# Kernel optimization log

Measured on AMD Instinct MI355X. Metric: run time of the kernel, lower is better.

Reference implementation:

```python
import jax, jax.numpy as jnp
import numpy as np

E = 8   # num_experts
K = 2   # top-k


def setup_inputs() -> dict:
    key = jax.random.key(0)
    ks = jax.random.split(key, 6)
    B, S, D, F = 4, 2048, 1024, 4096
    s_d = 1.0 / np.sqrt(D).astype(np.float32)
    s_f = 1.0 / np.sqrt(F).astype(np.float32)
    return {
        "x": jax.random.normal(ks[0], (B, S, D), jnp.float32),
        "ln_w": jnp.ones((D,), jnp.float32),                                 # RMSNorm weight
        "Wg": jax.random.normal(ks[1], (D, E), jnp.float32) * s_d,           # gating
        "bg": jnp.zeros((E,), jnp.float32),
        "W1a": jax.random.normal(ks[2], (E, D, F), jnp.float32) * s_d,       # stacked expert params
        "b1a": jnp.zeros((E, F), jnp.float32),
        "W1b": jax.random.normal(ks[3], (E, D, F), jnp.float32) * s_d,
        "b1b": jnp.zeros((E, F), jnp.float32),
        "W2": jax.random.normal(ks[4], (E, F, D), jnp.float32) * s_f,
        "b2": jnp.zeros((E, D), jnp.float32),
    }


def reference(x, ln_w, Wg, bg, W1a, b1a, W1b, b1b, W2, b2):
    B, S, D = x.shape
    eps = jnp.finfo(x.dtype).eps  # torch nn.RMSNorm default eps = finfo(dtype).eps
    # RMSNorm
    xn = x * jax.lax.rsqrt(jnp.mean(x * x, axis=-1, keepdims=True) + eps) * ln_w
    # gating -> top-k -> softmax over the k selected logits
    logits = xn @ Wg + bg                       # [B,S,E]
    vals, idx = jax.lax.top_k(logits, K)        # [B,S,K]
    topk_w = jax.nn.softmax(vals, axis=-1)      # [B,S,K]
    # combined per-expert gate weight per token (0 for unselected experts)
    we = jnp.sum(jax.nn.one_hot(idx, E, dtype=x.dtype) * topk_w[..., None], axis=-2)  # [B,S,E]

    T = B * S
    xf = xn.reshape(T, D)
    wef = we.reshape(T, E).T                    # [E,T], scanned per-expert

    def step(acc, params):
        W1a_e, b1a_e, W1b_e, b1b_e, W2_e, b2_e, w_e = params
        a = xf @ W1a_e + b1a_e                  # [T,F]
        b = xf @ W1b_e + b1b_e                  # [T,F]
        y = (jax.nn.silu(a) * b) @ W2_e + b2_e  # [T,D]
        return acc + w_e[:, None] * y, None

    out0 = jnp.zeros_like(xf)
    out, _ = jax.lax.scan(step, out0, (W1a, b1a, W1b, b1b, W2, b2, wef))
    return out.reshape(B, S, D)
```

## Files before the change

kernel.cpp:

```cpp
#include <hip/hip_runtime.h>
#include <hip/hip_bf16.h>
#include <cstdint>
#include <cstddef>

#define T_TOK 8192
#define DDIM  1024
#define FDIM  4096
#define NEXP  8
#define NSLOT (T_TOK*2)
#define BM    128
#define MAXTILE 136

typedef float  f32x4  __attribute__((ext_vector_type(4)));
typedef short  bf16x8 __attribute__((ext_vector_type(8)));
typedef unsigned short u16;

#define XN_OFF   ((size_t)0)
#define H_OFF    ((size_t)16777216)
#define META     ((size_t)(16777216+134217728))
#define CNT_OFF  (META + 0)
#define OFF_OFF  (META + 64)
#define NT_OFF   (META + 128)
#define TE_OFF   (META + 256)
#define TS_OFF   (META + 1024)
#define TR_OFF   (META + 1792)
#define EK_OFF   (META + 4096)
#define RK_OFF   (EK_OFF + 65536)
#define WK_OFF   (RK_OFF + 65536)
#define PT_OFF   (WK_OFF + 65536)
#define PW_OFF   (PT_OFF + 65536)
#define WT1A_OFF ((size_t)152 << 20)
#define WT1B_OFF (WT1A_OFF + ((size_t)64 << 20))
#define WT2_OFF  (WT1B_OFF + ((size_t)64 << 20))
#define WS_BIG   (WT2_OFF  + ((size_t)64 << 20))

__device__ __forceinline__ u16 f2bf(float f) {
    uint32_t x = __float_as_uint(f);
    x += 0x7fffu + ((x >> 16) & 1u);
    return (u16)(x >> 16);
}

__device__ __forceinline__ void gload_lds16(const u16* g, u16* l) {
    __builtin_amdgcn_global_load_lds(
        (const __attribute__((address_space(1))) unsigned int*)g,
        (__attribute__((address_space(3))) unsigned int*)l, 16, 0, 0);
}

__global__ __launch_bounds__(256) void k_rms_gate(
    const float* __restrict__ x, const float* __restrict__ lnw,
    const float* __restrict__ Wg, const float* __restrict__ bg,
    u16* __restrict__ xn, int* __restrict__ counts,
    int* __restrict__ ek, int* __restrict__ rk, float* __restrict__ wk)
{
    const int t = blockIdx.x;
    const int tid = threadIdx.x;
    const int wid = tid >> 6, lane = tid & 63;

    const float4 v = *(const float4*)(x + (size_t)t * DDIM + tid * 4);
    float ss = v.x * v.x + v.y * v.y + v.z * v.z + v.w * v.w;
    #pragma unroll
    for (int o = 32; o; o >>= 1) ss += __shfl_down(ss, o);

    __shared__ float s_red[4];
    __shared__ float s_lg[4][8];
    if (lane == 0) s_red[wid] = ss;
    __syncthreads();
    const float tot = s_red[0] + s_red[1] + s_red[2] + s_red[3];
    const float rms = rsqrtf(tot * (1.0f / DDIM) + 1.1920929e-7f);

    const float4 lw = *(const float4*)(lnw + tid * 4);
    float xv[4] = { v.x * rms * lw.x, v.y * rms * lw.y,
                    v.z * rms * lw.z, v.w * rms * lw.w };
    ushort4 xb;
    xb.x = f2bf(xv[0]); xb.y = f2bf(xv[1]); xb.z = f2bf(xv[2]); xb.w = f2bf(xv[3]);
    *(ushort4*)(xn + (size_t)t * DDIM + tid * 4) = xb;

    float lg[8];
    #pragma unroll
    for (int e = 0; e < 8; e++) lg[e] = 0.f;
    #pragma unroll
    for (int j = 0; j < 4; j++) {
        const float4 g0 = *(const float4*)(Wg + (size_t)(tid * 4 + j) * 8);
        const float4 g1 = *(const float4*)(Wg + (size_t)(tid * 4 + j) * 8 + 4);
        lg[0] += xv[j] * g0.x; lg[1] += xv[j] * g0.y;
        lg[2] += xv[j] * g0.z; lg[3] += xv[j] * g0.w;
        lg[4] += xv[j] * g1.x; lg[5] += xv[j] * g1.y;
        lg[6] += xv[j] * g1.z; lg[7] += xv[j] * g1.w;
    }
    #pragma unroll
    for (int e = 0; e < 8; e++) {
        #pragma unroll
        for (int o = 32; o; o >>= 1) lg[e] += __shfl_down(lg[e], o);
    }
    if (lane == 0) {
        #pragma unroll
        for (int e = 0; e < 8; e++) s_lg[wid][e] = lg[e];
    }
    __syncthreads();
    if (tid == 0) {
        float l[8];
        #pragma unroll
        for (int e = 0; e < 8; e++)
            l[e] = s_lg[0][e] + s_lg[1][e] + s_lg[2][e] + s_lg[3][e] + bg[e];
        int i0 = 0; float v0 = l[0];
        for (int e = 1; e < 8; e++) if (l[e] > v0) { v0 = l[e]; i0 = e; }
        int i1 = -1; float v1 = -3.4e38f;
        for (int e = 0; e < 8; e++) if (e != i0 && l[e] > v1) { v1 = l[e]; i1 = e; }
        const float w0 = 1.f / (1.f + __expf(v1 - v0));
        const float w1 = 1.f - w0;
        const int r0 = atomicAdd(&counts[i0], 1);
        const int r1 = atomicAdd(&counts[i1], 1);
        ek[t * 2]     = i0; rk[t * 2]     = r0; wk[t * 2]     = w0;
        ek[t * 2 + 1] = i1; rk[t * 2 + 1] = r1; wk[t * 2 + 1] = w1;
    }
}

__global__ void k_plan(const int* __restrict__ counts, int* __restrict__ offs,
                       int* __restrict__ ntile, int* __restrict__ tE,
                       int* __restrict__ tS, int* __restrict__ tR)
{
    if (threadIdx.x != 0 || blockIdx.x != 0) return;
    int off = 0, n = 0;
    for (int e = 0; e < NEXP; e++) {
        offs[e] = off;
        const int c = counts[e];
        for (int m = 0; m < c && n < MAXTILE; m += BM) {
            tE[n] = e; tS[n] = off + m; tR[n] = min(BM, c - m); n++;
        }
        off += c;
    }
    *ntile = n;
}

__global__ __launch_bounds__(256) void k_scatter(
    const int* __restrict__ ek, const int* __restrict__ rk,
    const float* __restrict__ wk, const int* __restrict__ offs,
    int* __restrict__ pt, float* __restrict__ pw)
{
    const int i = blockIdx.x * 256 + threadIdx.x;
    const int e = ek[i];
    const int slot = offs[e] + rk[i];
    pt[slot] = i >> 1;
    pw[slot] = wk[i];
}

__global__ __launch_bounds__(256) void k_transpose(
    const float* __restrict__ src, u16* __restrict__ dst, int R, int C)
{
    __shared__ u16 tile[64][72];
    const int e  = blockIdx.z;
    const int r0 = blockIdx.y * 64;
    const int c0 = blockIdx.x * 64;
    const int t  = threadIdx.x;
    const float* s = src + (size_t)e * R * C;
    u16* d         = dst + (size_t)e * R * C;

    const int lr = t >> 4;
    const int lc = (t & 15) * 4;
    #pragma unroll
    for (int i = 0; i < 4; i++) {
        const int r = lr + i * 16;
        const float4 v = *(const float4*)(s + (size_t)(r0 + r) * C + c0 + lc);
        tile[lc + 0][r] = f2bf(v.x);
        tile[lc + 1][r] = f2bf(v.y);
        tile[lc + 2][r] = f2bf(v.z);
        tile[lc + 3][r] = f2bf(v.w);
    }
    __syncthreads();
    const int wc = t >> 3;
    const int wr = (t & 7) * 8;
    #pragma unroll
    for (int i = 0; i < 2; i++) {
        const int c = wc + i * 32;
        const uint4 v = *(const uint4*)&tile[c][wr];
        *(uint4*)(d + (size_t)(c0 + c) * R + r0 + wr) = v;
    }
}

__global__ __launch_bounds__(256, 2) void k_gemm1_t(
    const u16* __restrict__ xn, const int* __restrict__ pt, const float* __restrict__ pw,
    const u16* __restrict__ wt1a, const float* __restrict__ b1a,
    const u16* __restrict__ wt1b, const float* __restrict__ b1b,
    const int* __restrict__ ntile, const int* __restrict__ tE,
    const int* __restrict__ tS, const int* __restrict__ tR,
    u16* __restrict__ h)
{
    const int bx = blockIdx.x;
    if (bx >= *ntile) return;
    const int e = tE[bx], slot0 = tS[bx], rows = tR[bx];
    const int f0 = blockIdx.y * 64;
    const int tid = threadIdx.x;

    __shared__ u16 lds[128 * 32 + 2 * 64 * 32];
    u16* ldsA  = lds;
    u16* ldsWa = lds + 128 * 32;
    u16* ldsWb = lds + 128 * 32 + 64 * 32;

    const int rA = tid >> 2, cA = tid & 3;
    const int tok0 = pt[slot0 + min(rA,      rows - 1)];
    const int tok1 = pt[slot0 + min(rA + 64, rows - 1)];
    const u16* gA0 = xn + (size_t)tok0 * DDIM + cA * 8;
    const u16* gA1 = xn + (size_t)tok1 * DDIM + cA * 8;
    const u16* gWa = wt1a + ((size_t)e * FDIM + f0 + rA) * DDIM + cA * 8;
    const u16* gWb = wt1b + ((size_t)e * FDIM + f0 + rA) * DDIM + cA * 8;
    u16* dA0 = ldsA  + tid * 8;
    u16* dA1 = ldsA  + 2048 + tid * 8;
    u16* dWa = ldsWa + tid * 8;
    u16* dWb = ldsWb + tid * 8;

    const int wid = tid >> 6, lane = tid & 63;
    const int wm = wid & 1, wn = wid >> 1;
    const int ln = lane & 15, q = lane >> 4;

    f32x4 accA[4][2], accB[4][2];
    #pragma unroll
    for (int i = 0; i < 4; i++)
        #pragma unroll
        for (int j = 0; j < 2; j++) {
            accA[i][j] = (f32x4){0.f, 0.f, 0.f, 0.f};
            accB[i][j] = (f32x4){0.f, 0.f, 0.f, 0.f};
        }

    for (int k0 = 0; k0 < DDIM; k0 += 32) {
        __syncthreads();
        gload_lds16(gA0 + k0, dA0);
        gload_lds16(gA1 + k0, dA1);
        gload_lds16(gWa + k0, dWa);
        gload_lds16(gWb + k0, dWb);
        __syncthreads();

        bf16x8 af[4], ba[2], bb[2];
        #pragma unroll
        for (int i = 0; i < 4; i++)
            af[i] = *(const bf16x8*)(ldsA + (wm * 64 + i * 16 + ln) * 32 + q * 8);
        #pragma unroll
        for (int j = 0; j < 2; j++) {
            ba[j] = *(const bf16x8*)(ldsWa + (wn * 32 + j * 16 + ln) * 32 + q * 8);
            bb[j] = *(const bf16x8*)(ldsWb + (wn * 32 + j * 16 + ln) * 32 + q * 8);
        }
        #pragma unroll
        for (int i = 0; i < 4; i++)
            #pragma unroll
            for (int j = 0; j < 2; j++) {
                accA[i][j] = __builtin_amdgcn_mfma_f32_16x16x32_bf16(af[i], ba[j], accA[i][j], 0, 0, 0);
                accB[i][j] = __builtin_amdgcn_mfma_f32_16x16x32_bf16(af[i], bb[j], accB[i][j], 0, 0, 0);
            }
    }

    #pragma unroll
    for (int i = 0; i < 4; i++) {
        const int mb = wm * 64 + i * 16 + q * 4;
        #pragma unroll
        for (int j = 0; j < 2; j++) {
            const int fg = f0 + wn * 32 + j * 16 + ln;
            const float bav = b1a[e * FDIM + fg];
            const float bbv = b1b[e * FDIM + fg];
            #pragma unroll
            for (int r = 0; r < 4; r++) {
                const int m = mb + r;
                if (m < rows) {
                    const float a = accA[i][j][r] + bav;
                    const float b = accB[i][j][r] + bbv;
                    const float s = a / (1.f + __expf(-a));
                    const float hv = pw[slot0 + m] * s * b;
                    h[(size_t)(slot0 + m) * FDIM + fg] = f2bf(hv);
                }
            }
        }
    }
}

__global__ __launch_bounds__(256, 2) void k_gemm2_t(
    const u16* __restrict__ h, const int* __restrict__ pt, const float* __restrict__ pw,
    const u16* __restrict__ wt2, const float* __restrict__ b2,
    const int* __restrict__ ntile, const int* __restrict__ tE,
    const int* __restrict__ tS, const int* __restrict__ tR,
    float* __restrict__ out)
{
    const int bx = blockIdx.x;
    if (bx >= *ntile) return;
    const int e = tE[bx], slot0 = tS[bx], rows = tR[bx];
    const int n0 = blockIdx.y * 128;
    const int tid = threadIdx.x;

    __shared__ u16 lds[2 * 128 * 32];
    u16* ldsA = lds;
    u16* ldsW = lds + 128 * 32;

    const int rA = tid >> 2, cA = tid & 3;
    const int r0c = min(rA,      rows - 1);
    const int r1c = min(rA + 64, rows - 1);
    const u16* gA0 = h + (size_t)(slot0 + r0c) * FDIM + cA * 8;
    const u16* gA1 = h + (size_t)(slot0 + r1c) * FDIM + cA * 8;
    const u16* gW0 = wt2 + ((size_t)e * DDIM + n0 + rA)      * FDIM + cA * 8;
    const u16* gW1 = wt2 + ((size_t)e * DDIM + n0 + rA + 64) * FDIM + cA * 8;
    u16* dA0 = ldsA + tid * 8;
    u16* dA1 = ldsA + 2048 + tid * 8;
    u16* dW0 = ldsW + tid * 8;
    u16* dW1 = ldsW + 2048 + tid * 8;

    const int wid = tid >> 6, lane = tid & 63;
    const int wm = wid & 1, wn = wid >> 1;
    const int ln = lane & 15, q = lane >> 4;

    f32x4 acc[4][4];
    #pragma unroll
    for (int i = 0; i < 4; i++)
        #pragma unroll
        for (int j = 0; j < 4; j++) acc[i][j] = (f32x4){0.f, 0.f, 0.f, 0.f};

    for (int k0 = 0; k0 < FDIM; k0 += 32) {
        __syncthreads();
        gload_lds16(gA0 + k0, dA0);
        gload_lds16(gA1 + k0, dA1);
        gload_lds16(gW0 + k0, dW0);
        gload_lds16(gW1 + k0, dW1);
        __syncthreads();

        bf16x8 af[4], bf[4];
        #pragma unroll
        for (int i = 0; i < 4; i++)
            af[i] = *(const bf16x8*)(ldsA + (wm * 64 + i * 16 + ln) * 32 + q * 8);
        #pragma unroll
        for (int j = 0; j < 4; j++)
            bf[j] = *(const bf16x8*)(ldsW + (wn * 64 + j * 16 + ln) * 32 + q * 8);
        #pragma unroll
        for (int i = 0; i < 4; i++)
            #pragma unroll
            for (int j = 0; j < 4; j++)
                acc[i][j] = __builtin_amdgcn_mfma_f32_16x16x32_bf16(af[i], bf[j], acc[i][j], 0, 0, 0);
    }

    #pragma unroll
    for (int i = 0; i < 4; i++) {
        const int mb = wm * 64 + i * 16 + q * 4;
        #pragma unroll
        for (int j = 0; j < 4; j++) {
            const int d = n0 + wn * 64 + j * 16 + ln;
            const float b2v = b2[e * DDIM + d];
            #pragma unroll
            for (int r = 0; r < 4; r++) {
                const int m = mb + r;
                if (m < rows) {
                    const int slot = slot0 + m;
                    const int tok = pt[slot];
                    const float val = acc[i][j][r] + pw[slot] * b2v;
                    atomicAdd(out + (size_t)tok * DDIM + d, val);
                }
            }
        }
    }
}


__global__ __launch_bounds__(256, 2) void k_gemm1(
    const u16* __restrict__ xn, const int* __restrict__ pt, const float* __restrict__ pw,
    const float* __restrict__ W1a, const float* __restrict__ b1a,
    const float* __restrict__ W1b, const float* __restrict__ b1b,
    const int* __restrict__ ntile, const int* __restrict__ tE,
    const int* __restrict__ tS, const int* __restrict__ tR,
    u16* __restrict__ h)
{
    const int bx = blockIdx.x;
    if (bx >= *ntile) return;
    const int e = tE[bx], slot0 = tS[bx], rows = tR[bx];
    const int f0 = blockIdx.y * 128;
    const int tid = threadIdx.x;

    __shared__ u16 lds[3 * 128 * 40];
    u16* ldsA  = lds;
    u16* ldsWa = lds + 128 * 40;
    u16* ldsWb = lds + 2 * 128 * 40;

    const int ar = tid >> 1, ah = tid & 1;
    const int tok = pt[slot0 + min(ar, rows - 1)];
    const u16* aptr = xn + (size_t)tok * DDIM + ah * 16;

    const int fq = tid & 31, dq = tid >> 5;
    const float* wa_base = W1a + (size_t)e * DDIM * FDIM + (f0 + fq * 4);
    const float* wb_base = W1b + (size_t)e * DDIM * FDIM + (f0 + fq * 4);

    const int wid = tid >> 6, lane = tid & 63;
    const int wm = wid & 1, wn = wid >> 1;
    const int ln = lane & 15, q = lane >> 4;

    f32x4 accA[4][4], accB[4][4];
    #pragma unroll
    for (int i = 0; i < 4; i++)
        #pragma unroll
        for (int j = 0; j < 4; j++) {
            accA[i][j] = (f32x4){0.f, 0.f, 0.f, 0.f};
            accB[i][j] = (f32x4){0.f, 0.f, 0.f, 0.f};
        }

    for (int k0 = 0; k0 < DDIM; k0 += 32) {
        const uint4 av0 = *(const uint4*)(aptr + k0);
        const uint4 av1 = *(const uint4*)(aptr + k0 + 8);
        float4 wa[4], wb[4];
        #pragma unroll
        for (int i = 0; i < 4; i++) {
            wa[i] = *(const float4*)(wa_base + (size_t)(k0 + dq * 4 + i) * FDIM);
            wb[i] = *(const float4*)(wb_base + (size_t)(k0 + dq * 4 + i) * FDIM);
        }
        __syncthreads();
        *(uint4*)(ldsA + ar * 40 + ah * 16)     = av0;
        *(uint4*)(ldsA + ar * 40 + ah * 16 + 8) = av1;
        #pragma unroll
        for (int j = 0; j < 4; j++) {
            ushort4 pa, pb;
            pa.x = f2bf(((const float*)&wa[0])[j]); pa.y = f2bf(((const float*)&wa[1])[j]);
            pa.z = f2bf(((const float*)&wa[2])[j]); pa.w = f2bf(((const float*)&wa[3])[j]);
            pb.x = f2bf(((const float*)&wb[0])[j]); pb.y = f2bf(((const float*)&wb[1])[j]);
            pb.z = f2bf(((const float*)&wb[2])[j]); pb.w = f2bf(((const float*)&wb[3])[j]);
            *(ushort4*)(ldsWa + (fq * 4 + j) * 40 + dq * 4) = pa;
            *(ushort4*)(ldsWb + (fq * 4 + j) * 40 + dq * 4) = pb;
        }
        __syncthreads();
        bf16x8 af[4], ba[4], bb[4];
        #pragma unroll
        for (int i = 0; i < 4; i++)
            af[i] = *(const bf16x8*)(ldsA + (wm * 64 + i * 16 + ln) * 40 + q * 8);
        #pragma unroll
        for (int j = 0; j < 4; j++) {
            ba[j] = *(const bf16x8*)(ldsWa + (wn * 64 + j * 16 + ln) * 40 + q * 8);
            bb[j] = *(const bf16x8*)(ldsWb + (wn * 64 + j * 16 + ln) * 40 + q * 8);
        }
        #pragma unroll
        for (int i = 0; i < 4; i++)
            #pragma unroll
            for (int j = 0; j < 4; j++) {
                accA[i][j] = __builtin_amdgcn_mfma_f32_16x16x32_bf16(af[i], ba[j], accA[i][j], 0, 0, 0);
                accB[i][j] = __builtin_amdgcn_mfma_f32_16x16x32_bf16(af[i], bb[j], accB[i][j], 0, 0, 0);
            }
    }

    #pragma unroll
    for (int i = 0; i < 4; i++) {
        const int mb = wm * 64 + i * 16 + q * 4;
        #pragma unroll
        for (int j = 0; j < 4; j++) {
            const int fg = f0 + wn * 64 + j * 16 + ln;
            const float bav = b1a[e * FDIM + fg];
            const float bbv = b1b[e * FDIM + fg];
            #pragma unroll
            for (int r = 0; r < 4; r++) {
                const int m = mb + r;
                if (m < rows) {
                    const float a = accA[i][j][r] + bav;
                    const float b = accB[i][j][r] + bbv;
                    const float s = a / (1.f + __expf(-a));
                    const float hv = pw[slot0 + m] * s * b;
                    h[(size_t)(slot0 + m) * FDIM + fg] = f2bf(hv);
                }
            }
        }
    }
}

__global__ __launch_bounds__(256, 2) void k_gemm2(
    const u16* __restrict__ h, const int* __restrict__ pt, const float* __restrict__ pw,
    const float* __restrict__ W2, const float* __restrict__ b2,
    const int* __restrict__ ntile, const int* __restrict__ tE,
    const int* __restrict__ tS, const int* __restrict__ tR,
    float* __restrict__ out)
{
    const int bx = blockIdx.x;
    if (bx >= *ntile) return;
    const int e = tE[bx], slot0 = tS[bx], rows = tR[bx];
    const int n0 = blockIdx.y * 128;
    const int tid = threadIdx.x;

    __shared__ u16 lds[2 * 128 * 40];
    u16* ldsA = lds;
    u16* ldsW = lds + 128 * 40;

    const int ar = tid >> 1, ah = tid & 1;
    const int arc = min(ar, rows - 1);
    const u16* aptr = h + (size_t)(slot0 + arc) * FDIM + ah * 16;

    const int fq = tid & 31, dq = tid >> 5;
    const float* w_base = W2 + (size_t)e * FDIM * DDIM + (n0 + fq * 4);

    const int wid = tid >> 6, lane = tid & 63;
    const int wm = wid & 1, wn = wid >> 1;
    const int ln = lane & 15, q = lane >> 4;

    f32x4 acc[4][4];
    #pragma unroll
    for (int i = 0; i < 4; i++)
        #pragma unroll
        for (int j = 0; j < 4; j++) acc[i][j] = (f32x4){0.f, 0.f, 0.f, 0.f};

    for (int k0 = 0; k0 < FDIM; k0 += 32) {
        const uint4 av0 = *(const uint4*)(aptr + k0);
        const uint4 av1 = *(const uint4*)(aptr + k0 + 8);
        float4 wv[4];
        #pragma unroll
        for (int i = 0; i < 4; i++)
            wv[i] = *(const float4*)(w_base + (size_t)(k0 + dq * 4 + i) * DDIM);
        __syncthreads();
        *(uint4*)(ldsA + ar * 40 + ah * 16)     = av0;
        *(uint4*)(ldsA + ar * 40 + ah * 16 + 8) = av1;
        #pragma unroll
        for (int j = 0; j < 4; j++) {
            ushort4 p;
            p.x = f2bf(((const float*)&wv[0])[j]); p.y = f2bf(((const float*)&wv[1])[j]);
            p.z = f2bf(((const float*)&wv[2])[j]); p.w = f2bf(((const float*)&wv[3])[j]);
            *(ushort4*)(ldsW + (fq * 4 + j) * 40 + dq * 4) = p;
        }
        __syncthreads();
        bf16x8 af[4], bf[4];
        #pragma unroll
        for (int i = 0; i < 4; i++)
            af[i] = *(const bf16x8*)(ldsA + (wm * 64 + i * 16 + ln) * 40 + q * 8);
        #pragma unroll
        for (int j = 0; j < 4; j++)
            bf[j] = *(const bf16x8*)(ldsW + (wn * 64 + j * 16 + ln) * 40 + q * 8);
        #pragma unroll
        for (int i = 0; i < 4; i++)
            #pragma unroll
            for (int j = 0; j < 4; j++)
                acc[i][j] = __builtin_amdgcn_mfma_f32_16x16x32_bf16(af[i], bf[j], acc[i][j], 0, 0, 0);
    }

    #pragma unroll
    for (int i = 0; i < 4; i++) {
        const int mb = wm * 64 + i * 16 + q * 4;
        #pragma unroll
        for (int j = 0; j < 4; j++) {
            const int d = n0 + wn * 64 + j * 16 + ln;
            const float b2v = b2[e * DDIM + d];
            #pragma unroll
            for (int r = 0; r < 4; r++) {
                const int m = mb + r;
                if (m < rows) {
                    const int slot = slot0 + m;
                    const int tok = pt[slot];
                    const float val = acc[i][j][r] + pw[slot] * b2v;
                    atomicAdd(out + (size_t)tok * DDIM + d, val);
                }
            }
        }
    }
}

extern "C" void kernel_launch(void* const* d_in, const int* in_sizes, int n_in,
                              void* d_out, int out_size, void* d_ws, size_t ws_size,
                              hipStream_t stream)
{
    (void)in_sizes; (void)n_in; (void)out_size;
    const float* x   = (const float*)d_in[0];
    const float* lnw = (const float*)d_in[1];
    const float* Wg  = (const float*)d_in[2];
    const float* bg  = (const float*)d_in[3];
    const float* W1a = (const float*)d_in[4];
    const float* b1a = (const float*)d_in[5];
    const float* W1b = (const float*)d_in[6];
    const float* b1b = (const float*)d_in[7];
    const float* W2  = (const float*)d_in[8];
    const float* b2  = (const float*)d_in[9];
    float* out = (float*)d_out;
    char* ws = (char*)d_ws;

    u16*   xn     = (u16*)(ws + XN_OFF);
    u16*   h      = (u16*)(ws + H_OFF);
    int*   counts = (int*)(ws + CNT_OFF);
    int*   offs   = (int*)(ws + OFF_OFF);
    int*   ntile  = (int*)(ws + NT_OFF);
    int*   tE     = (int*)(ws + TE_OFF);
    int*   tS     = (int*)(ws + TS_OFF);
    int*   tR     = (int*)(ws + TR_OFF);
    int*   ek     = (int*)(ws + EK_OFF);
    int*   rk     = (int*)(ws + RK_OFF);
    float* wk     = (float*)(ws + WK_OFF);
    int*   pt     = (int*)(ws + PT_OFF);
    float* pw     = (float*)(ws + PW_OFF);

    hipMemsetAsync(counts, 0, 32, stream);
    hipMemsetAsync(out, 0, (size_t)T_TOK * DDIM * sizeof(float), stream);

    const bool big = (ws_size >= WS_BIG);

    if (big) {
        u16* wt1a = (u16*)(ws + WT1A_OFF);
        u16* wt1b = (u16*)(ws + WT1B_OFF);
        u16* wt2  = (u16*)(ws + WT2_OFF);

        k_transpose<<<dim3(FDIM / 64, DDIM / 64, NEXP), 256, 0, stream>>>(W1a, wt1a, DDIM, FDIM);
        k_transpose<<<dim3(FDIM / 64, DDIM / 64, NEXP), 256, 0, stream>>>(W1b, wt1b, DDIM, FDIM);
        k_transpose<<<dim3(DDIM / 64, FDIM / 64, NEXP), 256, 0, stream>>>(W2,  wt2,  FDIM, DDIM);

        k_rms_gate<<<T_TOK, 256, 0, stream>>>(x, lnw, Wg, bg, xn, counts, ek, rk, wk);
        k_plan<<<1, 1, 0, stream>>>(counts, offs, ntile, tE, tS, tR);
        k_scatter<<<NSLOT / 256, 256, 0, stream>>>(ek, rk, wk, offs, pt, pw);

        dim3 g1(MAXTILE, FDIM / 64);
        k_gemm1_t<<<g1, 256, 0, stream>>>(xn, pt, pw, wt1a, b1a, wt1b, b1b,
                                          ntile, tE, tS, tR, h);
        dim3 g2(MAXTILE, DDIM / 128);
        k_gemm2_t<<<g2, 256, 0, stream>>>(h, pt, pw, wt2, b2,
                                          ntile, tE, tS, tR, out);
    } else {
        k_rms_gate<<<T_TOK, 256, 0, stream>>>(x, lnw, Wg, bg, xn, counts, ek, rk, wk);
        k_plan<<<1, 1, 0, stream>>>(counts, offs, ntile, tE, tS, tR);
        k_scatter<<<NSLOT / 256, 256, 0, stream>>>(ek, rk, wk, offs, pt, pw);

        dim3 g1(MAXTILE, FDIM / 128);
        k_gemm1<<<g1, 256, 0, stream>>>(xn, pt, pw, W1a, b1a, W1b, b1b,
                                        ntile, tE, tS, tR, h);
        dim3 g2(MAXTILE, DDIM / 128);
        k_gemm2<<<g2, 256, 0, stream>>>(h, pt, pw, W2, b2,
                                        ntile, tE, tS, tR, out);
    }
}
```

Before: 1.369 ms.

## Double N-tile width in both expert GEMMs and remap workgroups for XCD locality

Both transposed-weight expert GEMMs now compute wider output tiles: GEMM1 covers 128 F-columns per block for both W1a and W1b, and GEMM2 covers 256 D-columns. This raises arithmetic intensity per LDS load and halves how often the gathered activation rows are re-read. The block index is also remapped so consecutive hardware workgroups, which are dealt round-robin across 8 XCDs, process neighbouring tiles and share L2. Accumulator count doubles (64 and 32 f32x4 per thread), which risks register pressure and lower occupancy, and fewer blocks may underfill the device.

```diff
diff --git a/kernel.cpp b/kernel.cpp
--- a/kernel.cpp
+++ b/kernel.cpp
@@ -177,6 +177,7 @@
     }
 }
 
+#define G1_NWG (MAXTILE * (FDIM / 128))
 __global__ __launch_bounds__(256, 2) void k_gemm1_t(
     const u16* __restrict__ xn, const int* __restrict__ pt, const float* __restrict__ pw,
     const u16* __restrict__ wt1a, const float* __restrict__ b1a,
@@ -185,63 +186,72 @@
     const int* __restrict__ tS, const int* __restrict__ tR,
     u16* __restrict__ h)
 {
-    const int bx = blockIdx.x;
+    const int hw   = blockIdx.y * MAXTILE + blockIdx.x;
+    const int work = (hw & 7) * (G1_NWG / 8) + (hw >> 3);
+    const int bx   = work % MAXTILE;
+    const int f0   = (work / MAXTILE) * 128;
+
     if (bx >= *ntile) return;
     const int e = tE[bx], slot0 = tS[bx], rows = tR[bx];
-    const int f0 = blockIdx.y * 64;
     const int tid = threadIdx.x;
 
-    __shared__ u16 lds[128 * 32 + 2 * 64 * 32];
+    __shared__ u16 lds[3 * 128 * 32];
     u16* ldsA  = lds;
     u16* ldsWa = lds + 128 * 32;
-    u16* ldsWb = lds + 128 * 32 + 64 * 32;
+    u16* ldsWb = lds + 2 * 128 * 32;
 
     const int rA = tid >> 2, cA = tid & 3;
     const int tok0 = pt[slot0 + min(rA,      rows - 1)];
     const int tok1 = pt[slot0 + min(rA + 64, rows - 1)];
-    const u16* gA0 = xn + (size_t)tok0 * DDIM + cA * 8;
-    const u16* gA1 = xn + (size_t)tok1 * DDIM + cA * 8;
-    const u16* gWa = wt1a + ((size_t)e * FDIM + f0 + rA) * DDIM + cA * 8;
-    const u16* gWb = wt1b + ((size_t)e * FDIM + f0 + rA) * DDIM + cA * 8;
-    u16* dA0 = ldsA  + tid * 8;
-    u16* dA1 = ldsA  + 2048 + tid * 8;
-    u16* dWa = ldsWa + tid * 8;
-    u16* dWb = ldsWb + tid * 8;
+    const u16* gA0  = xn + (size_t)tok0 * DDIM + cA * 8;
+    const u16* gA1  = xn + (size_t)tok1 * DDIM + cA * 8;
+    const u16* gWa0 = wt1a + ((size_t)e * FDIM + f0 + rA) * DDIM + cA * 8;
+    const u16* gWa1 = gWa0 + (size_t)64 * DDIM;
+    const u16* gWb0 = wt1b + ((size_t)e * FDIM + f0 + rA) * DDIM + cA * 8;
+    const u16* gWb1 = gWb0 + (size_t)64 * DDIM;
+    u16* dA0  = ldsA  + tid * 8;
+    u16* dA1  = ldsA  + 2048 + tid * 8;
+    u16* dWa0 = ldsWa + tid * 8;
+    u16* dWa1 = ldsWa + 2048 + tid * 8;
+    u16* dWb0 = ldsWb + tid * 8;
+    u16* dWb1 = ldsWb + 2048 + tid * 8;
 
     const int wid = tid >> 6, lane = tid & 63;
     const int wm = wid & 1, wn = wid >> 1;
     const int ln = lane & 15, q = lane >> 4;
 
-    f32x4 accA[4][2], accB[4][2];
+    f32x4 accA[4][4], accB[4][4];
     #pragma unroll
     for (int i = 0; i < 4; i++)
         #pragma unroll
-        for (int j = 0; j < 2; j++) {
+        for (int j = 0; j < 4; j++) {
             accA[i][j] = (f32x4){0.f, 0.f, 0.f, 0.f};
             accB[i][j] = (f32x4){0.f, 0.f, 0.f, 0.f};
         }
 
     for (int k0 = 0; k0 < DDIM; k0 += 32) {
         __syncthreads();
-        gload_lds16(gA0 + k0, dA0);
-        gload_lds16(gA1 + k0, dA1);
-        gload_lds16(gWa + k0, dWa);
-        gload_lds16(gWb + k0, dWb);
-        __syncthreads();
-
-        bf16x8 af[4], ba[2], bb[2];
+        gload_lds16(gA0  + k0, dA0);
+        gload_lds16(gA1  + k0, dA1);
+        gload_lds16(gWa0 + k0, dWa0);
+        gload_lds16(gWa1 + k0, dWa1);
+        gload_lds16(gWb0 + k0, dWb0);
+        gload_lds16(gWb1 + k0, dWb1);
+        __syncthreads();
+
+        bf16x8 af[4], ba[4], bb[4];
         #pragma unroll
         for (int i = 0; i < 4; i++)
             af[i] = *(const bf16x8*)(ldsA + (wm * 64 + i * 16 + ln) * 32 + q * 8);
         #pragma unroll
-        for (int j = 0; j < 2; j++) {
-            ba[j] = *(const bf16x8*)(ldsWa + (wn * 32 + j * 16 + ln) * 32 + q * 8);
-            bb[j] = *(const bf16x8*)(ldsWb + (wn * 32 + j * 16 + ln) * 32 + q * 8);
-        }
-        #pragma unroll
-        for (int i = 0; i < 4; i++)
-            #pragma unroll
-            for (int j = 0; j < 2; j++) {
+        for (int j = 0; j < 4; j++) {
+            ba[j] = *(const bf16x8*)(ldsWa + (wn * 64 + j * 16 + ln) * 32 + q * 8);
+            bb[j] = *(const bf16x8*)(ldsWb + (wn * 64 + j * 16 + ln) * 32 + q * 8);
+        }
+        #pragma unroll
+        for (int i = 0; i < 4; i++)
+            #pragma unroll
+            for (int j = 0; j < 4; j++) {
                 accA[i][j] = __builtin_amdgcn_mfma_f32_16x16x32_bf16(af[i], ba[j], accA[i][j], 0, 0, 0);
                 accB[i][j] = __builtin_amdgcn_mfma_f32_16x16x32_bf16(af[i], bb[j], accB[i][j], 0, 0, 0);
             }
@@ -251,8 +261,8 @@
     for (int i = 0; i < 4; i++) {
         const int mb = wm * 64 + i * 16 + q * 4;
         #pragma unroll
-        for (int j = 0; j < 2; j++) {
-            const int fg = f0 + wn * 32 + j * 16 + ln;
+        for (int j = 0; j < 4; j++) {
+            const int fg = f0 + wn * 64 + j * 16 + ln;
             const float bav = b1a[e * FDIM + fg];
             const float bbv = b1b[e * FDIM + fg];
             #pragma unroll
@@ -270,6 +280,7 @@
     }
 }
 
+#define G2_NWG (MAXTILE * (DDIM / 256))
 __global__ __launch_bounds__(256, 2) void k_gemm2_t(
     const u16* __restrict__ h, const int* __restrict__ pt, const float* __restrict__ pw,
     const u16* __restrict__ wt2, const float* __restrict__ b2,
@@ -277,13 +288,16 @@
     const int* __restrict__ tS, const int* __restrict__ tR,
     float* __restrict__ out)
 {
-    const int bx = blockIdx.x;
+    const int hw   = blockIdx.y * MAXTILE + blockIdx.x;
+    const int work = (hw & 7) * (G2_NWG / 8) + (hw >> 3);
+    const int bx   = work % MAXTILE;
+    const int n0   = (work / MAXTILE) * 256;
+
     if (bx >= *ntile) return;
     const int e = tE[bx], slot0 = tS[bx], rows = tR[bx];
-    const int n0 = blockIdx.y * 128;
     const int tid = threadIdx.x;
 
-    __shared__ u16 lds[2 * 128 * 32];
+    __shared__ u16 lds[128 * 32 + 256 * 32];
     u16* ldsA = lds;
     u16* ldsW = lds + 128 * 32;
 
@@ -292,22 +306,26 @@
     const int r1c = min(rA + 64, rows - 1);
     const u16* gA0 = h + (size_t)(slot0 + r0c) * FDIM + cA * 8;
     const u16* gA1 = h + (size_t)(slot0 + r1c) * FDIM + cA * 8;
-    const u16* gW0 = wt2 + ((size_t)e * DDIM + n0 + rA)      * FDIM + cA * 8;
-    const u16* gW1 = wt2 + ((size_t)e * DDIM + n0 + rA + 64) * FDIM + cA * 8;
+    const u16* gW0 = wt2 + ((size_t)e * DDIM + n0 + rA)       * FDIM + cA * 8;
+    const u16* gW1 = gW0 + (size_t)64  * FDIM;
+    const u16* gW2 = gW0 + (size_t)128 * FDIM;
+    const u16* gW3 = gW0 + (size_t)192 * FDIM;
     u16* dA0 = ldsA + tid * 8;
     u16* dA1 = ldsA + 2048 + tid * 8;
     u16* dW0 = ldsW + tid * 8;
     u16* dW1 = ldsW + 2048 + tid * 8;
+    u16* dW2 = ldsW + 4096 + tid * 8;
+    u16* dW3 = ldsW + 6144 + tid * 8;
 
     const int wid = tid >> 6, lane = tid & 63;
     const int wm = wid & 1, wn = wid >> 1;
     const int ln = lane & 15, q = lane >> 4;
 
-    f32x4 acc[4][4];
+    f32x4 acc[4][8];
     #pragma unroll
     for (int i = 0; i < 4; i++)
         #pragma unroll
-        for (int j = 0; j < 4; j++) acc[i][j] = (f32x4){0.f, 0.f, 0.f, 0.f};
+        for (int j = 0; j < 8; j++) acc[i][j] = (f32x4){0.f, 0.f, 0.f, 0.f};
 
     for (int k0 = 0; k0 < FDIM; k0 += 32) {
         __syncthreads();
@@ -315,19 +333,21 @@
         gload_lds16(gA1 + k0, dA1);
         gload_lds16(gW0 + k0, dW0);
         gload_lds16(gW1 + k0, dW1);
-        __syncthreads();
-
-        bf16x8 af[4], bf[4];
+        gload_lds16(gW2 + k0, dW2);
+        gload_lds16(gW3 + k0, dW3);
+        __syncthreads();
+
+        bf16x8 af[4], bf[8];
         #pragma unroll
         for (int i = 0; i < 4; i++)
             af[i] = *(const bf16x8*)(ldsA + (wm * 64 + i * 16 + ln) * 32 + q * 8);
         #pragma unroll
-        for (int j = 0; j < 4; j++)
-            bf[j] = *(const bf16x8*)(ldsW + (wn * 64 + j * 16 + ln) * 32 + q * 8);
-        #pragma unroll
-        for (int i = 0; i < 4; i++)
-            #pragma unroll
-            for (int j = 0; j < 4; j++)
+        for (int j = 0; j < 8; j++)
+            bf[j] = *(const bf16x8*)(ldsW + (wn * 128 + j * 16 + ln) * 32 + q * 8);
+        #pragma unroll
+        for (int i = 0; i < 4; i++)
+            #pragma unroll
+            for (int j = 0; j < 8; j++)
                 acc[i][j] = __builtin_amdgcn_mfma_f32_16x16x32_bf16(af[i], bf[j], acc[i][j], 0, 0, 0);
     }
 
@@ -335,8 +355,8 @@
     for (int i = 0; i < 4; i++) {
         const int mb = wm * 64 + i * 16 + q * 4;
         #pragma unroll
-        for (int j = 0; j < 4; j++) {
-            const int d = n0 + wn * 64 + j * 16 + ln;
+        for (int j = 0; j < 8; j++) {
+            const int d = n0 + wn * 128 + j * 16 + ln;
             const float b2v = b2[e * DDIM + d];
             #pragma unroll
             for (int r = 0; r < 4; r++) {
@@ -594,10 +614,10 @@
         k_plan<<<1, 1, 0, stream>>>(counts, offs, ntile, tE, tS, tR);
         k_scatter<<<NSLOT / 256, 256, 0, stream>>>(ek, rk, wk, offs, pt, pw);
 
-        dim3 g1(MAXTILE, FDIM / 64);
+        dim3 g1(MAXTILE, FDIM / 128);
         k_gemm1_t<<<g1, 256, 0, stream>>>(xn, pt, pw, wt1a, b1a, wt1b, b1b,
                                           ntile, tE, tS, tR, h);
-        dim3 g2(MAXTILE, DDIM / 128);
+        dim3 g2(MAXTILE, DDIM / 256);
         k_gemm2_t<<<g2, 256, 0, stream>>>(h, pt, pw, wt2, b2,
                                           ntile, tE, tS, tR, out);
     } else {
```

Result: slower. 1.464 ms (+7.0%).

## Double K-step per barrier and remap workgroups across XCDs in expert GEMMs

Applied to the files above, without the earlier changes.

Both expert GEMM kernels now load a 64-wide K slab into LDS per iteration as two 32-wide sub-tiles. This halves the number of __syncthreads pairs and issues more loads in flight per barrier. The launch index is also remapped so that consecutive hardware workgroup ids, which are spread round-robin over the 8 XCDs, map to contiguous work items, improving L2 locality of shared weight and activation tiles. The cost is double the LDS per block, which may reduce occupancy.

```diff
diff --git a/kernel.cpp b/kernel.cpp
--- a/kernel.cpp
+++ b/kernel.cpp
@@ -177,6 +177,7 @@
     }
 }
 
+#define G1_NWG (MAXTILE * (FDIM / 64))
 __global__ __launch_bounds__(256, 2) void k_gemm1_t(
     const u16* __restrict__ xn, const int* __restrict__ pt, const float* __restrict__ pw,
     const u16* __restrict__ wt1a, const float* __restrict__ b1a,
@@ -185,16 +186,19 @@
     const int* __restrict__ tS, const int* __restrict__ tR,
     u16* __restrict__ h)
 {
-    const int bx = blockIdx.x;
+    const int hw   = blockIdx.y * MAXTILE + blockIdx.x;
+    const int work = (hw & 7) * (G1_NWG / 8) + (hw >> 3);
+    const int bx   = work % MAXTILE;
+    const int f0   = (work / MAXTILE) * 64;
+
     if (bx >= *ntile) return;
     const int e = tE[bx], slot0 = tS[bx], rows = tR[bx];
-    const int f0 = blockIdx.y * 64;
     const int tid = threadIdx.x;
 
-    __shared__ u16 lds[128 * 32 + 2 * 64 * 32];
+    __shared__ u16 lds[128 * 64 + 2 * 64 * 64];
     u16* ldsA  = lds;
-    u16* ldsWa = lds + 128 * 32;
-    u16* ldsWb = lds + 128 * 32 + 64 * 32;
+    u16* ldsWa = lds + 128 * 64;
+    u16* ldsWb = lds + 128 * 64 + 64 * 64;
 
     const int rA = tid >> 2, cA = tid & 3;
     const int tok0 = pt[slot0 + min(rA,      rows - 1)];
@@ -203,10 +207,14 @@
     const u16* gA1 = xn + (size_t)tok1 * DDIM + cA * 8;
     const u16* gWa = wt1a + ((size_t)e * FDIM + f0 + rA) * DDIM + cA * 8;
     const u16* gWb = wt1b + ((size_t)e * FDIM + f0 + rA) * DDIM + cA * 8;
-    u16* dA0 = ldsA  + tid * 8;
-    u16* dA1 = ldsA  + 2048 + tid * 8;
-    u16* dWa = ldsWa + tid * 8;
-    u16* dWb = ldsWb + tid * 8;
+    u16* dA00 = ldsA  + tid * 8;
+    u16* dA01 = ldsA  + 2048 + tid * 8;
+    u16* dA10 = ldsA  + 4096 + tid * 8;
+    u16* dA11 = ldsA  + 6144 + tid * 8;
+    u16* dWa0 = ldsWa + tid * 8;
+    u16* dWa1 = ldsWa + 2048 + tid * 8;
+    u16* dWb0 = ldsWb + tid * 8;
+    u16* dWb1 = ldsWb + 2048 + tid * 8;
 
     const int wid = tid >> 6, lane = tid & 63;
     const int wm = wid & 1, wn = wid >> 1;
@@ -221,30 +229,37 @@
             accB[i][j] = (f32x4){0.f, 0.f, 0.f, 0.f};
         }
 
-    for (int k0 = 0; k0 < DDIM; k0 += 32) {
-        __syncthreads();
-        gload_lds16(gA0 + k0, dA0);
-        gload_lds16(gA1 + k0, dA1);
-        gload_lds16(gWa + k0, dWa);
-        gload_lds16(gWb + k0, dWb);
-        __syncthreads();
-
-        bf16x8 af[4], ba[2], bb[2];
-        #pragma unroll
-        for (int i = 0; i < 4; i++)
-            af[i] = *(const bf16x8*)(ldsA + (wm * 64 + i * 16 + ln) * 32 + q * 8);
-        #pragma unroll
-        for (int j = 0; j < 2; j++) {
-            ba[j] = *(const bf16x8*)(ldsWa + (wn * 32 + j * 16 + ln) * 32 + q * 8);
-            bb[j] = *(const bf16x8*)(ldsWb + (wn * 32 + j * 16 + ln) * 32 + q * 8);
-        }
-        #pragma unroll
-        for (int i = 0; i < 4; i++)
+    for (int k0 = 0; k0 < DDIM; k0 += 64) {
+        __syncthreads();
+        gload_lds16(gA0 + k0,      dA00);
+        gload_lds16(gA1 + k0,      dA01);
+        gload_lds16(gA0 + k0 + 32, dA10);
+        gload_lds16(gA1 + k0 + 32, dA11);
+        gload_lds16(gWa + k0,      dWa0);
+        gload_lds16(gWa + k0 + 32, dWa1);
+        gload_lds16(gWb + k0,      dWb0);
+        gload_lds16(gWb + k0 + 32, dWb1);
+        __syncthreads();
+
+        #pragma unroll
+        for (int s = 0; s < 2; s++) {
+            bf16x8 af[4], ba[2], bb[2];
+            #pragma unroll
+            for (int i = 0; i < 4; i++)
+                af[i] = *(const bf16x8*)(ldsA + s * 4096 + (wm * 64 + i * 16 + ln) * 32 + q * 8);
             #pragma unroll
             for (int j = 0; j < 2; j++) {
-                accA[i][j] = __builtin_amdgcn_mfma_f32_16x16x32_bf16(af[i], ba[j], accA[i][j], 0, 0, 0);
-                accB[i][j] = __builtin_amdgcn_mfma_f32_16x16x32_bf16(af[i], bb[j], accB[i][j], 0, 0, 0);
+                ba[j] = *(const bf16x8*)(ldsWa + s * 2048 + (wn * 32 + j * 16 + ln) * 32 + q * 8);
+                bb[j] = *(const bf16x8*)(ldsWb + s * 2048 + (wn * 32 + j * 16 + ln) * 32 + q * 8);
             }
+            #pragma unroll
+            for (int i = 0; i < 4; i++)
+                #pragma unroll
+                for (int j = 0; j < 2; j++) {
+                    accA[i][j] = __builtin_amdgcn_mfma_f32_16x16x32_bf16(af[i], ba[j], accA[i][j], 0, 0, 0);
+                    accB[i][j] = __builtin_amdgcn_mfma_f32_16x16x32_bf16(af[i], bb[j], accB[i][j], 0, 0, 0);
+                }
+        }
     }
 
     #pragma unroll
@@ -270,6 +285,7 @@
     }
 }
 
+#define G2_NWG (MAXTILE * (DDIM / 128))
 __global__ __launch_bounds__(256, 2) void k_gemm2_t(
     const u16* __restrict__ h, const int* __restrict__ pt, const float* __restrict__ pw,
     const u16* __restrict__ wt2, const float* __restrict__ b2,
@@ -277,15 +293,18 @@
     const int* __restrict__ tS, const int* __restrict__ tR,
     float* __restrict__ out)
 {
-    const int bx = blockIdx.x;
+    const int hw   = blockIdx.y * MAXTILE + blockIdx.x;
+    const int work = (hw & 7) * (G2_NWG / 8) + (hw >> 3);
+    const int bx   = work % MAXTILE;
+    const int n0   = (work / MAXTILE) * 128;
+
     if (bx >= *ntile) return;
     const int e = tE[bx], slot0 = tS[bx], rows = tR[bx];
-    const int n0 = blockIdx.y * 128;
     const int tid = threadIdx.x;
 
-    __shared__ u16 lds[2 * 128 * 32];
+    __shared__ u16 lds[2 * 128 * 64];
     u16* ldsA = lds;
-    u16* ldsW = lds + 128 * 32;
+    u16* ldsW = lds + 128 * 64;
 
     const int rA = tid >> 2, cA = tid & 3;
     const int r0c = min(rA,      rows - 1);
@@ -294,10 +313,14 @@
     const u16* gA1 = h + (size_t)(slot0 + r1c) * FDIM + cA * 8;
     const u16* gW0 = wt2 + ((size_t)e * DDIM + n0 + rA)      * FDIM + cA * 8;
     const u16* gW1 = wt2 + ((size_t)e * DDIM + n0 + rA + 64) * FDIM + cA * 8;
-    u16* dA0 = ldsA + tid * 8;
-    u16* dA1 = ldsA + 2048 + tid * 8;
-    u16* dW0 = ldsW + tid * 8;
-    u16* dW1 = ldsW + 2048 + tid * 8;
+    u16* dA00 = ldsA + tid * 8;
+    u16* dA01 = ldsA + 2048 + tid * 8;
+    u16* dA10 = ldsA + 4096 + tid * 8;
+    u16* dA11 = ldsA + 6144 + tid * 8;
+    u16* dW00 = ldsW + tid * 8;
+    u16* dW01 = ldsW + 2048 + tid * 8;
+    u16* dW10 = ldsW + 4096 + tid * 8;
+    u16* dW11 = ldsW + 6144 + tid * 8;
 
     const int wid = tid >> 6, lane = tid & 63;
     const int wm = wid & 1, wn = wid >> 1;
@@ -309,26 +332,33 @@
         #pragma unroll
         for (int j = 0; j < 4; j++) acc[i][j] = (f32x4){0.f, 0.f, 0.f, 0.f};
 
-    for (int k0 = 0; k0 < FDIM; k0 += 32) {
-        __syncthreads();
-        gload_lds16(gA0 + k0, dA0);
-        gload_lds16(gA1 + k0, dA1);
-        gload_lds16(gW0 + k0, dW0);
-        gload_lds16(gW1 + k0, dW1);
-        __syncthreads();
-
-        bf16x8 af[4], bf[4];
-        #pragma unroll
-        for (int i = 0; i < 4; i++)
-            af[i] = *(const bf16x8*)(ldsA + (wm * 64 + i * 16 + ln) * 32 + q * 8);
-        #pragma unroll
-        for (int j = 0; j < 4; j++)
-            bf[j] = *(const bf16x8*)(ldsW + (wn * 64 + j * 16 + ln) * 32 + q * 8);
-        #pragma unroll
-        for (int i = 0; i < 4; i++)
+    for (int k0 = 0; k0 < FDIM; k0 += 64) {
+        __syncthreads();
+        gload_lds16(gA0 + k0,      dA00);
+        gload_lds16(gA1 + k0,      dA01);
+        gload_lds16(gA0 + k0 + 32, dA10);
+        gload_lds16(gA1 + k0 + 32, dA11);
+        gload_lds16(gW0 + k0,      dW00);
+        gload_lds16(gW1 + k0,      dW01);
+        gload_lds16(gW0 + k0 + 32, dW10);
+        gload_lds16(gW1 + k0 + 32, dW11);
+        __syncthreads();
+
+        #pragma unroll
+        for (int s = 0; s < 2; s++) {
+            bf16x8 af[4], bf[4];
+            #pragma unroll
+            for (int i = 0; i < 4; i++)
+                af[i] = *(const bf16x8*)(ldsA + s * 4096 + (wm * 64 + i * 16 + ln) * 32 + q * 8);
             #pragma unroll
             for (int j = 0; j < 4; j++)
-                acc[i][j] = __builtin_amdgcn_mfma_f32_16x16x32_bf16(af[i], bf[j], acc[i][j], 0, 0, 0);
+                bf[j] = *(const bf16x8*)(ldsW + s * 4096 + (wn * 64 + j * 16 + ln) * 32 + q * 8);
+            #pragma unroll
+            for (int i = 0; i < 4; i++)
+                #pragma unroll
+                for (int j = 0; j < 4; j++)
+                    acc[i][j] = __builtin_amdgcn_mfma_f32_16x16x32_bf16(af[i], bf[j], acc[i][j], 0, 0, 0);
+        }
     }
 
     #pragma unroll
```

After: 1.253 ms. 8.4% less time.
